# Kernel tuning notes

Measured on AMD Instinct MI355X. Metric: run time of the kernel, lower is better.

## Reference

```python
import jax, jax.numpy as jnp
import numpy as np

B, S, I, H = 32, 512, 512, 1024

def _xavier(key, shape):
    fan_in, fan_out = shape[0], shape[1]
    a = jnp.sqrt(6.0 / (fan_in + fan_out))
    return jax.random.uniform(key, shape, jnp.float32, -a, a)

def setup_inputs() -> dict:
    key = jax.random.key(0)
    ks = jax.random.split(key, 10)
    inp = {
        'x': jax.random.normal(ks[0], (B, S, I), jnp.float32),
        'h0': jnp.zeros((B, H), jnp.float32),
        'c0': jnp.zeros((B, H), jnp.float32),
        'W_ii': _xavier(ks[1], (I, H)), 'W_hi': _xavier(ks[2], (H, H)), 'b_i': jnp.zeros((H,), jnp.float32),
        'W_if': _xavier(ks[3], (I, H)), 'W_hf': _xavier(ks[4], (H, H)), 'b_f': jnp.zeros((H,), jnp.float32),
        'W_ig': _xavier(ks[5], (I, H)), 'W_hg': _xavier(ks[6], (H, H)), 'b_g': jnp.zeros((H,), jnp.float32),
        'W_io': _xavier(ks[7], (I, H)), 'W_ho': _xavier(ks[8], (H, H)), 'b_o': jnp.zeros((H,), jnp.float32),
    }
    return inp

def _lstm(x, h0, c0, W_ii, W_hi, b_i, W_if, W_hf, b_f, W_ig, W_hg, b_g, W_io, W_ho, b_o):
    # Precompute input-to-hidden projections for all timesteps (big fused GEMMs).
    xi = jnp.einsum('bsi,ih->sbh', x, W_ii) + b_i  # (S,B,H)
    xf = jnp.einsum('bsi,ih->sbh', x, W_if) + b_f
    xg = jnp.einsum('bsi,ih->sbh', x, W_ig) + b_g
    xo = jnp.einsum('bsi,ih->sbh', x, W_io) + b_o

    def step(carry, gates_t):
        h, c = carry
        xi_t, xf_t, xg_t, xo_t = gates_t
        i_t = jax.nn.sigmoid(xi_t + h @ W_hi)
        f_t = jax.nn.sigmoid(xf_t + h @ W_hf)
        g_t = jnp.tanh(xg_t + h @ W_hg)
        o_t = jax.nn.sigmoid(xo_t + h @ W_ho)
        c_new = f_t * c + i_t * g_t
        h_new = o_t * jnp.tanh(c_new)
        return (h_new, c_new), (h_new, f_t, i_t, o_t, g_t, c_new)

    (hT, cT), (hs, fs, is_, os, gs, cs) = jax.lax.scan(step, (h0, c0), (xi, xf, xg, xo))
    hidden_seq = jnp.transpose(hs, (1, 0, 2))  # (B,S,H)
    return hidden_seq, hT, cT, fs, is_, os, gs, cs

def reference(x, h0, c0, W_ii, W_hi, b_i, W_if, W_hf, b_f, W_ig, W_hg, b_g, W_io, W_ho, b_o):
    return _lstm(x, h0, c0, W_ii, W_hi, b_i, W_if, W_hf, b_f, W_ig, W_hg, b_g, W_io, W_ho, b_o)
```

## Files before the change

kernel.cpp:

```cpp
#include <hip/hip_runtime.h>
#include <stdint.h>

#define S_LEN 512
#define BATCH 32
#define IDIM 512
#define HDIM 1024
#define NBLK 64

typedef __attribute__((ext_vector_type(8))) short bf16x8;
typedef __attribute__((ext_vector_type(4))) float f32x4;

typedef const __attribute__((address_space(1))) unsigned int as1_uint;
typedef __attribute__((address_space(3))) unsigned int as3_uint;

__device__ __forceinline__ unsigned short f2bf(float f) {
  unsigned int u = __float_as_uint(f);
  u = (u + 0x7fffu + ((u >> 16) & 1u)) >> 16;
  return (unsigned short)u;
}

__device__ __forceinline__ void gld_lds16(const void* g, void* l) {
  __builtin_amdgcn_global_load_lds((as1_uint*)g, (as3_uint*)l, 16, 0, 0);
}

__device__ __forceinline__ float sigm(float x) { return 1.f / (1.f + __expf(-x)); }
__device__ __forceinline__ float tanh_f(float x) { return 1.f - 2.f / (__expf(2.f * x) + 1.f); }

__global__ void k_cast_x(const float* __restrict__ src, unsigned short* __restrict__ dst, int n8) {
  int i0 = blockIdx.x * blockDim.x + threadIdx.x;
  int stride = gridDim.x * blockDim.x;
  for (int i = i0; i < n8; i += stride) {
    const float4* s4 = (const float4*)(src + (size_t)i * 8);
    float4 a = s4[0], b = s4[1];
    bf16x8 v;
    v[0] = (short)f2bf(a.x); v[1] = (short)f2bf(a.y); v[2] = (short)f2bf(a.z); v[3] = (short)f2bf(a.w);
    v[4] = (short)f2bf(b.x); v[5] = (short)f2bf(b.y); v[6] = (short)f2bf(b.z); v[7] = (short)f2bf(b.w);
    *(bf16x8*)(dst + (size_t)i * 8) = v;
  }
}

__global__ void k_tcast_w(const float* __restrict__ src, unsigned short* __restrict__ dst, int K) {
  __shared__ float t[64][65];
  int k0 = blockIdx.x * 64, h0 = blockIdx.y * 64;
  int tid = threadIdx.x;
#pragma unroll 4
  for (int j = 0; j < 16; ++j) {
    int idx = j * 256 + tid;
    int kl = idx >> 6, hl = idx & 63;
    t[kl][hl] = src[(size_t)(k0 + kl) * HDIM + h0 + hl];
  }
  __syncthreads();
  int hl = tid >> 2, kg = tid & 3;
  unsigned short* drow = dst + (size_t)(h0 + hl) * K + k0 + kg * 16;
#pragma unroll
  for (int jj = 0; jj < 4; ++jj) {
    ushort4 v;
    v.x = f2bf(t[kg * 16 + jj * 4 + 0][hl]);
    v.y = f2bf(t[kg * 16 + jj * 4 + 1][hl]);
    v.z = f2bf(t[kg * 16 + jj * 4 + 2][hl]);
    v.w = f2bf(t[kg * 16 + jj * 4 + 3][hl]);
    *(ushort4*)(drow + jj * 4) = v;
  }
}

__global__ __launch_bounds__(256) void k_proj(
    const unsigned short* __restrict__ xb, const unsigned short* __restrict__ wib,
    const float* __restrict__ b_i, const float* __restrict__ b_f,
    const float* __restrict__ b_g, const float* __restrict__ b_o,
    float* __restrict__ Xi, float* __restrict__ Xf, float* __restrict__ Xg,
    float* __restrict__ Xo) {
  __shared__ unsigned short As[128 * 64];
  __shared__ unsigned short Bs[128 * 64];
  int tid = threadIdx.x;
  int l = tid & 63, w = tid >> 6;
  int mt = blockIdx.x >> 5, nt = blockIdx.x & 31;
  int m0 = mt * 128, n0 = nt * 128;
  int g = nt >> 3;
  int wm = (w >> 1) * 64, wn = (w & 1) * 64;

  f32x4 acc[4][4];
  for (int mi = 0; mi < 4; ++mi)
    for (int ni = 0; ni < 4; ++ni)
      for (int r = 0; r < 4; ++r) acc[mi][ni][r] = 0.f;

  for (int kt = 0; kt < 8; ++kt) {
    int k0 = kt * 64;
#pragma unroll
    for (int j = 0; j < 4; ++j) {
      int idx = j * 256 + tid;
      int row = idx >> 3, c = idx & 7;
      int sc = c ^ (row & 7);
      gld_lds16(xb + (size_t)(m0 + row) * IDIM + k0 + sc * 8,
                (char*)As + ((j * 256 + (w << 6)) << 4));
      gld_lds16(wib + (size_t)(n0 + row) * IDIM + k0 + sc * 8,
                (char*)Bs + ((j * 256 + (w << 6)) << 4));
    }
    __syncthreads();
#pragma unroll
    for (int kst = 0; kst < 2; ++kst) {
      bf16x8 af[4], bfr[4];
#pragma unroll
      for (int mi = 0; mi < 4; ++mi) {
        int row = wm + mi * 16 + (l & 15);
        int c = (kst << 2) + (l >> 4);
        af[mi] = *(const bf16x8*)((const char*)As + row * 128 + ((c ^ (row & 7)) << 4));
      }
#pragma unroll
      for (int ni = 0; ni < 4; ++ni) {
        int row = wn + ni * 16 + (l & 15);
        int c = (kst << 2) + (l >> 4);
        bfr[ni] = *(const bf16x8*)((const char*)Bs + row * 128 + ((c ^ (row & 7)) << 4));
      }
#pragma unroll
      for (int mi = 0; mi < 4; ++mi)
#pragma unroll
        for (int ni = 0; ni < 4; ++ni)
          acc[mi][ni] = __builtin_amdgcn_mfma_f32_16x16x32_bf16(af[mi], bfr[ni], acc[mi][ni], 0, 0, 0);
    }
    __syncthreads();
  }

  const float* bias = g == 0 ? b_i : g == 1 ? b_f : g == 2 ? b_g : b_o;
  float* dst = g == 0 ? Xi : g == 1 ? Xf : g == 2 ? Xg : Xo;
#pragma unroll
  for (int ni = 0; ni < 4; ++ni) {
    int n = n0 + wn + ni * 16 + (l & 15);
    int h = n & 1023;
    float bv = bias[h];
#pragma unroll
    for (int mi = 0; mi < 4; ++mi)
#pragma unroll
      for (int r = 0; r < 4; ++r) {
        int m = m0 + wm + mi * 16 + ((l >> 4) << 2) + r;
        int b = m >> 9, s = m & 511;
        dst[(size_t)(s * BATCH + b) * HDIM + h] = acc[mi][ni][r] + bv;
      }
  }
}

__global__ __launch_bounds__(256, 1) void k_rnn(
    const unsigned short* __restrict__ whb, const float* __restrict__ h0,
    const float* __restrict__ c0, char* __restrict__ hbufA,
    char* __restrict__ hbufB, unsigned int* __restrict__ cnt,
    const float* __restrict__ Xi, const float* __restrict__ Xf,
    const float* __restrict__ Xg, const float* __restrict__ Xo,
    float* __restrict__ csw, float* __restrict__ hseq, float* __restrict__ hT,
    float* __restrict__ cT) {
  __shared__ char lds[41472];
  const int ACT = 32768;

  const int tid = threadIdx.x;
  const int w = tid >> 6, l = tid & 63;
  const int ln = l & 15, lk = l >> 4;
  const int bid = blockIdx.x;
  const int dm = bid & 1, hb = bid >> 1;

  float* isw = (float*)Xi; float* fsw = (float*)Xf;
  float* gsw = (float*)Xg; float* osw = (float*)Xo;
  const float* XW = (w == 0) ? Xi : (w == 1) ? Xf : (w == 2) ? Xg : Xo;

  bf16x8 Breg[8][8];
#pragma unroll
  for (int g = 0; g < 4; ++g)
#pragma unroll
    for (int hh = 0; hh < 2; ++hh)
#pragma unroll
      for (int j = 0; j < 8; ++j) {
        const size_t row = (size_t)((g << 10) + (hb << 5) + (hh << 4) + ln);
        Breg[g * 2 + hh][j] =
            *(const bf16x8*)(whb + (row << 10) + (w << 8) + (j << 5) + (lk << 3));
      }
#pragma unroll
  for (int nt = 0; nt < 8; ++nt)
#pragma unroll
    for (int j = 0; j < 8; ++j)
      asm volatile("" : "+a"(Breg[nt][j]));

  const int pb = tid >> 4, hp = tid & 15;
  const int bg = (dm << 4) + pb;
  const int gh = (hb << 5) + (hp << 1);
  const int o = hp << 1;
  const int foff = (dm << 15) + (hb << 10) + ((o >> 3) << 8) + (pb << 4) + ((o & 7) << 1);
  unsigned int* const myflag = cnt + (((dm << 2) + (hb & 3)) << 5);

  float2 c = *(const float2*)&c0[((size_t)bg << 10) + gh];

  {
    float2 hv = *(const float2*)&h0[((size_t)bg << 10) + gh];
    unsigned int pv = (unsigned int)f2bf(hv.x) | ((unsigned int)f2bf(hv.y) << 16);
    __hip_atomic_store((unsigned int*)(hbufA + foff), pv, __ATOMIC_RELAXED,
                       __HIP_MEMORY_SCOPE_AGENT);
    asm volatile("s_waitcnt vmcnt(0)" ::: "memory");
    __syncthreads();
    if (tid == 0)
      __hip_atomic_fetch_add(myflag, 1u, __ATOMIC_RELAXED, __HIP_MEMORY_SCOPE_AGENT);
  }

  for (int t = 0; t < S_LEN; ++t) {
    const char* hin = (t & 1) ? hbufB : hbufA;
    char* hout = (t & 1) ? hbufA : hbufB;

    float xp[2][4];
    {
      const float* xb_ = XW + ((size_t)((t << 5) + (dm << 4)) << 10) + (hb << 5) + ln;
#pragma unroll
      for (int hh = 0; hh < 2; ++hh)
#pragma unroll
        for (int r = 0; r < 4; ++r)
          xp[hh][r] = xb_[((size_t)((lk << 2) + r) << 10) + (hh << 4)];
    }

    {
      const unsigned int need = 8u * (unsigned int)(t + 1);
      const unsigned int* cp = cnt + (((dm << 2) + (l & 3)) << 5);
      while (true) {
        unsigned int v = __hip_atomic_load(cp, __ATOMIC_RELAXED, __HIP_MEMORY_SCOPE_AGENT);
        if (__all((l < 4) ? (int)(v >= need) : 1)) break;
        __builtin_amdgcn_s_sleep(1);
      }
    }
    __builtin_amdgcn_sched_barrier(0);

    bf16x8 a[8];
    const char* abase = hin + (dm << 15);
#pragma unroll
    for (int j = 0; j < 8; ++j) {
      const char* ap = abase + (((w << 3) + j) << 10) + (l << 4);
      asm volatile("global_load_dwordx4 %0, %1, off sc0 sc1"
                   : "=v"(a[j]) : "v"(ap) : "memory");
    }
    asm volatile("s_waitcnt vmcnt(0)" ::: "memory");
    __builtin_amdgcn_sched_barrier(0);

    f32x4 acc[8];
#pragma unroll
    for (int nt = 0; nt < 8; ++nt)
#pragma unroll
      for (int r = 0; r < 4; ++r) acc[nt][r] = 0.f;
#pragma unroll
    for (int j = 0; j < 8; ++j)
#pragma unroll
      for (int nt = 0; nt < 8; ++nt)
        acc[nt] = __builtin_amdgcn_mfma_f32_16x16x32_bf16(a[j], Breg[nt][j], acc[nt], 0, 0, 0);

#pragma unroll
    for (int nt = 0; nt < 8; ++nt)
      *(f32x4*)(lds + (((w << 3) + nt) << 10) + (l << 4)) = acc[nt];
    __syncthreads();

#pragma unroll
    for (int hh = 0; hh < 2; ++hh) {
      const int nt = (w << 1) + hh;
      f32x4 s = *(const f32x4*)(lds + (nt << 10) + (l << 4));
#pragma unroll
      for (int kw = 1; kw < 4; ++kw) {
        f32x4 p = *(const f32x4*)(lds + (((kw << 3) + nt) << 10) + (l << 4));
#pragma unroll
        for (int r = 0; r < 4; ++r) s[r] += p[r];
      }
#pragma unroll
      for (int r = 0; r < 4; ++r) {
        float pre = s[r] + xp[hh][r];
        float act = (w == 2) ? tanh_f(pre) : sigm(pre);
        ((float*)(lds + ACT))[((w << 4) + (lk << 2) + r) * 34 + (hh << 4) + ln] = act;
      }
    }
    __syncthreads();

    const float* af = (const float*)(lds + ACT);
    float2 iv = *(const float2*)&af[(0 * 16 + pb) * 34 + o];
    float2 fv = *(const float2*)&af[(1 * 16 + pb) * 34 + o];
    float2 gv = *(const float2*)&af[(2 * 16 + pb) * 34 + o];
    float2 ov = *(const float2*)&af[(3 * 16 + pb) * 34 + o];

    c.x = fv.x * c.x + iv.x * gv.x;
    c.y = fv.y * c.y + iv.y * gv.y;
    float h0v = ov.x * tanh_f(c.x), h1v = ov.y * tanh_f(c.y);

    if (t < S_LEN - 1) {
      unsigned int pv = (unsigned int)f2bf(h0v) | ((unsigned int)f2bf(h1v) << 16);
      __hip_atomic_store((unsigned int*)(hout + foff), pv, __ATOMIC_RELAXED,
                         __HIP_MEMORY_SCOPE_AGENT);
      asm volatile("s_waitcnt vmcnt(0)" ::: "memory");
      __syncthreads();
      if (tid == 0)
        __hip_atomic_fetch_add(myflag, 1u, __ATOMIC_RELAXED, __HIP_MEMORY_SCOPE_AGENT);
    }

    size_t oo = ((size_t)((t << 5) + bg) << 10) + gh;
    *(float2*)(isw + oo) = iv;
    *(float2*)(fsw + oo) = fv;
    *(float2*)(gsw + oo) = gv;
    *(float2*)(osw + oo) = ov;
    *(float2*)(csw + oo) = c;
    *(float2*)(hseq + (((size_t)(bg << 9) + t) << 10) + gh) = make_float2(h0v, h1v);
    if (t == S_LEN - 1) {
      *(float2*)(hT + ((size_t)bg << 10) + gh) = make_float2(h0v, h1v);
      *(float2*)(cT + ((size_t)bg << 10) + gh) = c;
    }
  }
}

extern "C" void kernel_launch(void* const* d_in, const int* in_sizes, int n_in,
                              void* d_out, int out_size, void* d_ws, size_t ws_size,
                              hipStream_t stream) {
  const float* x = (const float*)d_in[0];
  const float* h0 = (const float*)d_in[1];
  const float* c0 = (const float*)d_in[2];
  const float* Wi[4] = {(const float*)d_in[3], (const float*)d_in[6], (const float*)d_in[9], (const float*)d_in[12]};
  const float* Wh[4] = {(const float*)d_in[4], (const float*)d_in[7], (const float*)d_in[10], (const float*)d_in[13]};
  const float* bias[4] = {(const float*)d_in[5], (const float*)d_in[8], (const float*)d_in[11], (const float*)d_in[14]};

  float* out = (float*)d_out;
  float* R0 = out;
  float* R1 = out + 16777216;
  float* R2 = R1 + 32768;
  float* R3 = R2 + 32768;
  float* R4 = R3 + 16777216;
  float* R5 = R4 + 16777216;
  float* R6 = R5 + 16777216;
  float* R7 = R6 + 16777216;
  float* Xg_[4] = {R4, R3, R6, R5};

  char* ws = (char*)d_ws;
  unsigned short* whb = (unsigned short*)ws;
  unsigned short* wib = (unsigned short*)(ws + 8388608);
  char* hbufA = ws + 12582912;
  char* hbufB = ws + 12648448;
  unsigned int* cnt = (unsigned int*)(ws + 12713984);

  unsigned short* xb = (unsigned short*)R0;

  hipMemsetAsync(cnt, 0, 1024, stream);
  k_cast_x<<<2048, 256, 0, stream>>>(x, xb, (BATCH * S_LEN * IDIM) / 8);
  for (int g = 0; g < 4; ++g) {
    k_tcast_w<<<dim3(8, 16), 256, 0, stream>>>(Wi[g], wib + (size_t)g * 1024 * 512, 512);
    k_tcast_w<<<dim3(16, 16), 256, 0, stream>>>(Wh[g], whb + (size_t)g * 1024 * 1024, 1024);
  }
  k_proj<<<4096, 256, 0, stream>>>(xb, wib, bias[0], bias[1], bias[2], bias[3],
                                   Xg_[0], Xg_[1], Xg_[2], Xg_[3]);
  k_rnn<<<NBLK, 256, 0, stream>>>(whb, h0, c0, hbufA, hbufB, cnt,
                                  Xg_[0], Xg_[1], Xg_[2], Xg_[3],
                                  R7, R0, R1, R2);
}
```

Measured before the change: 1.945 ms.

## Replace counter-flag barrier with tagged hidden-state publishing for step sync

Each thread now writes its bf16 hidden pair together with a 32-bit step tag in a single 64-bit atomic store. Consumers spin by reloading the whole h slice and checking the tags, so the data load also serves as the readiness check. This removes the per-block s_waitcnt, __syncthreads, atomic counter increment and separate polling loop on the recurrent critical path. In exchange each step moves twice the h data and consumers repeatedly reload the full slice while waiting. The hx buffer reuses the wib region in the workspace and is cleared after the projection kernel has finished with it.

```diff
diff --git a/kernel.cpp b/kernel.cpp
--- a/kernel.cpp
+++ b/kernel.cpp
@@ -6,9 +6,11 @@
 #define IDIM 512
 #define HDIM 1024
 #define NBLK 64
+#define TAGB 0xC0DE0000u
 
 typedef __attribute__((ext_vector_type(8))) short bf16x8;
 typedef __attribute__((ext_vector_type(4))) float f32x4;
+typedef __attribute__((ext_vector_type(4))) unsigned int u32x4;
 
 typedef const __attribute__((address_space(1))) unsigned int as1_uint;
 typedef __attribute__((address_space(3))) unsigned int as3_uint;
@@ -25,6 +27,10 @@
 
 __device__ __forceinline__ float sigm(float x) { return 1.f / (1.f + __expf(-x)); }
 __device__ __forceinline__ float tanh_f(float x) { return 1.f - 2.f / (__expf(2.f * x) + 1.f); }
+
+#define LDX4(dst, addr, OFF)                                             \
+  asm volatile("global_load_dwordx4 %0, %1, off offset:" #OFF " sc0 sc1" \
+               : "=v"(dst) : "v"(addr) : "memory")
 
 __global__ void k_cast_x(const float* __restrict__ src, unsigned short* __restrict__ dst, int n8) {
   int i0 = blockIdx.x * blockDim.x + threadIdx.x;
@@ -140,8 +146,7 @@
 
 __global__ __launch_bounds__(256, 1) void k_rnn(
     const unsigned short* __restrict__ whb, const float* __restrict__ h0,
-    const float* __restrict__ c0, char* __restrict__ hbufA,
-    char* __restrict__ hbufB, unsigned int* __restrict__ cnt,
+    const float* __restrict__ c0, char* __restrict__ hx,
     const float* __restrict__ Xi, const float* __restrict__ Xf,
     const float* __restrict__ Xg, const float* __restrict__ Xo,
     float* __restrict__ csw, float* __restrict__ hseq, float* __restrict__ hT,
@@ -180,26 +185,21 @@
   const int bg = (dm << 4) + pb;
   const int gh = (hb << 5) + (hp << 1);
   const int o = hp << 1;
-  const int foff = (dm << 15) + (hb << 10) + ((o >> 3) << 8) + (pb << 4) + ((o & 7) << 1);
-  unsigned int* const myflag = cnt + (((dm << 2) + (hb & 3)) << 5);
+  char* const pub = hx + (dm << 16) + (pb << 12) + (((hb << 4) + hp) << 3);
+  const char* const cons = hx + (dm << 16) + (ln << 12) + (w << 10) + (lk << 5);
 
   float2 c = *(const float2*)&c0[((size_t)bg << 10) + gh];
 
   {
     float2 hv = *(const float2*)&h0[((size_t)bg << 10) + gh];
-    unsigned int pv = (unsigned int)f2bf(hv.x) | ((unsigned int)f2bf(hv.y) << 16);
-    __hip_atomic_store((unsigned int*)(hbufA + foff), pv, __ATOMIC_RELAXED,
+    unsigned long long pv =
+        (unsigned long long)((unsigned int)f2bf(hv.x) | ((unsigned int)f2bf(hv.y) << 16)) |
+        ((unsigned long long)TAGB << 32);
+    __hip_atomic_store((unsigned long long*)pub, pv, __ATOMIC_RELAXED,
                        __HIP_MEMORY_SCOPE_AGENT);
-    asm volatile("s_waitcnt vmcnt(0)" ::: "memory");
-    __syncthreads();
-    if (tid == 0)
-      __hip_atomic_fetch_add(myflag, 1u, __ATOMIC_RELAXED, __HIP_MEMORY_SCOPE_AGENT);
   }
 
   for (int t = 0; t < S_LEN; ++t) {
-    const char* hin = (t & 1) ? hbufB : hbufA;
-    char* hout = (t & 1) ? hbufA : hbufB;
-
     float xp[2][4];
     {
       const float* xb_ = XW + ((size_t)((t << 5) + (dm << 4)) << 10) + (hb << 5) + ln;
@@ -210,27 +210,35 @@
           xp[hh][r] = xb_[((size_t)((lk << 2) + r) << 10) + (hh << 4)];
     }
 
-    {
-      const unsigned int need = 8u * (unsigned int)(t + 1);
-      const unsigned int* cp = cnt + (((dm << 2) + (l & 3)) << 5);
-      while (true) {
-        unsigned int v = __hip_atomic_load(cp, __ATOMIC_RELAXED, __HIP_MEMORY_SCOPE_AGENT);
-        if (__all((l < 4) ? (int)(v >= need) : 1)) break;
-        __builtin_amdgcn_s_sleep(1);
-      }
-    }
-    __builtin_amdgcn_sched_barrier(0);
+    const char* ab = cons + ((t & 1) << 17);
+    const unsigned int want = TAGB + (unsigned int)t;
+    u32x4 raw[16];
+    while (true) {
+      LDX4(raw[0], ab, 0);    LDX4(raw[1], ab, 16);
+      LDX4(raw[2], ab, 128);  LDX4(raw[3], ab, 144);
+      LDX4(raw[4], ab, 256);  LDX4(raw[5], ab, 272);
+      LDX4(raw[6], ab, 384);  LDX4(raw[7], ab, 400);
+      LDX4(raw[8], ab, 512);  LDX4(raw[9], ab, 528);
+      LDX4(raw[10], ab, 640); LDX4(raw[11], ab, 656);
+      LDX4(raw[12], ab, 768); LDX4(raw[13], ab, 784);
+      LDX4(raw[14], ab, 896); LDX4(raw[15], ab, 912);
+      asm volatile("s_waitcnt vmcnt(0)" ::: "memory");
+      __builtin_amdgcn_sched_barrier(0);
+      unsigned int ok = 1;
+#pragma unroll
+      for (int i = 0; i < 16; ++i)
+        ok &= (unsigned int)(raw[i][1] == want) & (unsigned int)(raw[i][3] == want);
+      if (__all((int)ok)) break;
+    }
 
     bf16x8 a[8];
-    const char* abase = hin + (dm << 15);
 #pragma unroll
     for (int j = 0; j < 8; ++j) {
-      const char* ap = abase + (((w << 3) + j) << 10) + (l << 4);
-      asm volatile("global_load_dwordx4 %0, %1, off sc0 sc1"
-                   : "=v"(a[j]) : "v"(ap) : "memory");
-    }
-    asm volatile("s_waitcnt vmcnt(0)" ::: "memory");
-    __builtin_amdgcn_sched_barrier(0);
+      u32x4 t4;
+      t4[0] = raw[2 * j][0]; t4[1] = raw[2 * j][2];
+      t4[2] = raw[2 * j + 1][0]; t4[3] = raw[2 * j + 1][2];
+      a[j] = __builtin_bit_cast(bf16x8, t4);
+    }
 
     f32x4 acc[8];
 #pragma unroll
@@ -278,13 +286,11 @@
     float h0v = ov.x * tanh_f(c.x), h1v = ov.y * tanh_f(c.y);
 
     if (t < S_LEN - 1) {
-      unsigned int pv = (unsigned int)f2bf(h0v) | ((unsigned int)f2bf(h1v) << 16);
-      __hip_atomic_store((unsigned int*)(hout + foff), pv, __ATOMIC_RELAXED,
-                         __HIP_MEMORY_SCOPE_AGENT);
-      asm volatile("s_waitcnt vmcnt(0)" ::: "memory");
-      __syncthreads();
-      if (tid == 0)
-        __hip_atomic_fetch_add(myflag, 1u, __ATOMIC_RELAXED, __HIP_MEMORY_SCOPE_AGENT);
+      unsigned long long pv =
+          (unsigned long long)((unsigned int)f2bf(h0v) | ((unsigned int)f2bf(h1v) << 16)) |
+          ((unsigned long long)(TAGB + (unsigned int)(t + 1)) << 32);
+      __hip_atomic_store((unsigned long long*)(pub + ((~t & 1) << 17)), pv,
+                         __ATOMIC_RELAXED, __HIP_MEMORY_SCOPE_AGENT);
     }
 
     size_t oo = ((size_t)((t << 5) + bg) << 10) + gh;
@@ -325,13 +331,10 @@
   char* ws = (char*)d_ws;
   unsigned short* whb = (unsigned short*)ws;
   unsigned short* wib = (unsigned short*)(ws + 8388608);
-  char* hbufA = ws + 12582912;
-  char* hbufB = ws + 12648448;
-  unsigned int* cnt = (unsigned int*)(ws + 12713984);
+  char* hx = ws + 8388608;
 
   unsigned short* xb = (unsigned short*)R0;
 
-  hipMemsetAsync(cnt, 0, 1024, stream);
   k_cast_x<<<2048, 256, 0, stream>>>(x, xb, (BATCH * S_LEN * IDIM) / 8);
   for (int g = 0; g < 4; ++g) {
     k_tcast_w<<<dim3(8, 16), 256, 0, stream>>>(Wi[g], wib + (size_t)g * 1024 * 512, 512);
@@ -339,7 +342,8 @@
   }
   k_proj<<<4096, 256, 0, stream>>>(xb, wib, bias[0], bias[1], bias[2], bias[3],
                                    Xg_[0], Xg_[1], Xg_[2], Xg_[3]);
-  k_rnn<<<NBLK, 256, 0, stream>>>(whb, h0, c0, hbufA, hbufB, cnt,
+  hipMemsetAsync(hx, 0, 262144, stream);
+  k_rnn<<<NBLK, 256, 0, stream>>>(whb, h0, c0, hx,
                                   Xg_[0], Xg_[1], Xg_[2], Xg_[3],
                                   R7, R0, R1, R2);
 }
```

Result: slower. 2.687 ms (+38.2%).

## Signal per-wave readiness and defer per-step output stores past the h fetch

Applied to the files above, without the earlier changes.

Drops the block-wide barrier before signalling that h is ready. Each wave now bumps the ready counter itself after its own store completes, and the wait threshold rises from 8 to 32 per step to match. The gate and state output stores for step t are deferred into step t+1, issued after the h operand loads, and the XW prefetch moves after them. The aim is to take the output write traffic and the barrier off the recurrent critical path. In exchange there are four times as many atomic increments per step, and the vmcnt(0) waits may now cover the deferred stores.

```diff
diff --git a/kernel.cpp b/kernel.cpp
--- a/kernel.cpp
+++ b/kernel.cpp
@@ -185,14 +185,16 @@
 
   float2 c = *(const float2*)&c0[((size_t)bg << 10) + gh];
 
+  float2 piv, pfv, pgv, pov, pc;
+  float ph0 = 0.f, ph1 = 0.f;
+
   {
     float2 hv = *(const float2*)&h0[((size_t)bg << 10) + gh];
     unsigned int pv = (unsigned int)f2bf(hv.x) | ((unsigned int)f2bf(hv.y) << 16);
     __hip_atomic_store((unsigned int*)(hbufA + foff), pv, __ATOMIC_RELAXED,
                        __HIP_MEMORY_SCOPE_AGENT);
     asm volatile("s_waitcnt vmcnt(0)" ::: "memory");
-    __syncthreads();
-    if (tid == 0)
+    if (l == 0)
       __hip_atomic_fetch_add(myflag, 1u, __ATOMIC_RELAXED, __HIP_MEMORY_SCOPE_AGENT);
   }
 
@@ -200,18 +202,8 @@
     const char* hin = (t & 1) ? hbufB : hbufA;
     char* hout = (t & 1) ? hbufA : hbufB;
 
-    float xp[2][4];
     {
-      const float* xb_ = XW + ((size_t)((t << 5) + (dm << 4)) << 10) + (hb << 5) + ln;
-#pragma unroll
-      for (int hh = 0; hh < 2; ++hh)
-#pragma unroll
-        for (int r = 0; r < 4; ++r)
-          xp[hh][r] = xb_[((size_t)((lk << 2) + r) << 10) + (hh << 4)];
-    }
-
-    {
-      const unsigned int need = 8u * (unsigned int)(t + 1);
+      const unsigned int need = 32u * (unsigned int)(t + 1);
       const unsigned int* cp = cnt + (((dm << 2) + (l & 3)) << 5);
       while (true) {
         unsigned int v = __hip_atomic_load(cp, __ATOMIC_RELAXED, __HIP_MEMORY_SCOPE_AGENT);
@@ -232,6 +224,26 @@
     asm volatile("s_waitcnt vmcnt(0)" ::: "memory");
     __builtin_amdgcn_sched_barrier(0);
 
+    if (t > 0) {
+      size_t po = ((size_t)(((t - 1) << 5) + bg) << 10) + gh;
+      *(float2*)(isw + po) = piv;
+      *(float2*)(fsw + po) = pfv;
+      *(float2*)(gsw + po) = pgv;
+      *(float2*)(osw + po) = pov;
+      *(float2*)(csw + po) = pc;
+      *(float2*)(hseq + (((size_t)(bg << 9) + (t - 1)) << 10) + gh) = make_float2(ph0, ph1);
+    }
+
+    float xp[2][4];
+    {
+      const float* xb_ = XW + ((size_t)((t << 5) + (dm << 4)) << 10) + (hb << 5) + ln;
+#pragma unroll
+      for (int hh = 0; hh < 2; ++hh)
+#pragma unroll
+        for (int r = 0; r < 4; ++r)
+          xp[hh][r] = xb_[((size_t)((lk << 2) + r) << 10) + (hh << 4)];
+    }
+
     f32x4 acc[8];
 #pragma unroll
     for (int nt = 0; nt < 8; ++nt)
@@ -282,22 +294,23 @@
       __hip_atomic_store((unsigned int*)(hout + foff), pv, __ATOMIC_RELAXED,
                          __HIP_MEMORY_SCOPE_AGENT);
       asm volatile("s_waitcnt vmcnt(0)" ::: "memory");
-      __syncthreads();
-      if (tid == 0)
+      if (l == 0)
         __hip_atomic_fetch_add(myflag, 1u, __ATOMIC_RELAXED, __HIP_MEMORY_SCOPE_AGENT);
     }
 
-    size_t oo = ((size_t)((t << 5) + bg) << 10) + gh;
-    *(float2*)(isw + oo) = iv;
-    *(float2*)(fsw + oo) = fv;
-    *(float2*)(gsw + oo) = gv;
-    *(float2*)(osw + oo) = ov;
-    *(float2*)(csw + oo) = c;
-    *(float2*)(hseq + (((size_t)(bg << 9) + t) << 10) + gh) = make_float2(h0v, h1v);
-    if (t == S_LEN - 1) {
-      *(float2*)(hT + ((size_t)bg << 10) + gh) = make_float2(h0v, h1v);
-      *(float2*)(cT + ((size_t)bg << 10) + gh) = c;
-    }
+    piv = iv; pfv = fv; pgv = gv; pov = ov; pc = c; ph0 = h0v; ph1 = h1v;
+  }
+
+  {
+    size_t po = ((size_t)(((S_LEN - 1) << 5) + bg) << 10) + gh;
+    *(float2*)(isw + po) = piv;
+    *(float2*)(fsw + po) = pfv;
+    *(float2*)(gsw + po) = pgv;
+    *(float2*)(osw + po) = pov;
+    *(float2*)(csw + po) = pc;
+    *(float2*)(hseq + (((size_t)(bg << 9) + (S_LEN - 1)) << 10) + gh) = make_float2(ph0, ph1);
+    *(float2*)(hT + ((size_t)bg << 10) + gh) = make_float2(ph0, ph1);
+    *(float2*)(cT + ((size_t)bg << 10) + gh) = pc;
   }
 }
 
```

Result: slower. 2.372 ms (+21.9%).

## Replace atomic counters with per-block step flags and pipeline h loads into MFMAs

Applied to the files above, without the earlier changes.

Each block now stores its own step number into a dedicated slot instead of doing atomic fetch-adds on 4 shared counters, and every lane of a wave polls one flag. This is meant to remove atomic contention and shorten the cross-block barrier in the recurrent loop. The h-vector loads are also drained incrementally with staged vmcnt waits, so MFMAs for early chunks start before later loads arrive. The x-projection loads become inline asm so they are not reordered. The risk is that the vmcnt counting now depends on the exact ordering of outstanding loads, including the asm x loads issued earlier.

```diff
diff --git a/kernel.cpp b/kernel.cpp
--- a/kernel.cpp
+++ b/kernel.cpp
@@ -141,7 +141,7 @@
 __global__ __launch_bounds__(256, 1) void k_rnn(
     const unsigned short* __restrict__ whb, const float* __restrict__ h0,
     const float* __restrict__ c0, char* __restrict__ hbufA,
-    char* __restrict__ hbufB, unsigned int* __restrict__ cnt,
+    char* __restrict__ hbufB, unsigned int* __restrict__ sent,
     const float* __restrict__ Xi, const float* __restrict__ Xf,
     const float* __restrict__ Xg, const float* __restrict__ Xo,
     float* __restrict__ csw, float* __restrict__ hseq, float* __restrict__ hT,
@@ -181,7 +181,8 @@
   const int gh = (hb << 5) + (hp << 1);
   const int o = hp << 1;
   const int foff = (dm << 15) + (hb << 10) + ((o >> 3) << 8) + (pb << 4) + ((o & 7) << 1);
-  unsigned int* const myflag = cnt + (((dm << 2) + (hb & 3)) << 5);
+  unsigned int* const smy = sent + (dm << 7) + ((hb >> 3) << 5) + ((hb & 7) << 2);
+  const unsigned int* const spoll = sent + (dm << 7) + (w << 5) + ((l & 7) << 2);
 
   float2 c = *(const float2*)&c0[((size_t)bg << 10) + gh];
 
@@ -193,7 +194,7 @@
     asm volatile("s_waitcnt vmcnt(0)" ::: "memory");
     __syncthreads();
     if (tid == 0)
-      __hip_atomic_fetch_add(myflag, 1u, __ATOMIC_RELAXED, __HIP_MEMORY_SCOPE_AGENT);
+      __hip_atomic_store(smy, 1u, __ATOMIC_RELAXED, __HIP_MEMORY_SCOPE_AGENT);
   }
 
   for (int t = 0; t < S_LEN; ++t) {
@@ -206,16 +207,18 @@
 #pragma unroll
       for (int hh = 0; hh < 2; ++hh)
 #pragma unroll
-        for (int r = 0; r < 4; ++r)
-          xp[hh][r] = xb_[((size_t)((lk << 2) + r) << 10) + (hh << 4)];
+        for (int r = 0; r < 4; ++r) {
+          const float* xa = xb_ + (((size_t)((lk << 2) + r)) << 10) + (hh << 4);
+          asm volatile("global_load_dword %0, %1, off"
+                       : "=v"(xp[hh][r]) : "v"(xa) : "memory");
+        }
     }
 
     {
-      const unsigned int need = 8u * (unsigned int)(t + 1);
-      const unsigned int* cp = cnt + (((dm << 2) + (l & 3)) << 5);
+      const unsigned int need = (unsigned int)(t + 1);
       while (true) {
-        unsigned int v = __hip_atomic_load(cp, __ATOMIC_RELAXED, __HIP_MEMORY_SCOPE_AGENT);
-        if (__all((l < 4) ? (int)(v >= need) : 1)) break;
+        unsigned int v = __hip_atomic_load(spoll, __ATOMIC_RELAXED, __HIP_MEMORY_SCOPE_AGENT);
+        if (__all((int)(v >= need))) break;
         __builtin_amdgcn_s_sleep(1);
       }
     }
@@ -229,19 +232,26 @@
       asm volatile("global_load_dwordx4 %0, %1, off sc0 sc1"
                    : "=v"(a[j]) : "v"(ap) : "memory");
     }
-    asm volatile("s_waitcnt vmcnt(0)" ::: "memory");
-    __builtin_amdgcn_sched_barrier(0);
-
     f32x4 acc[8];
 #pragma unroll
     for (int nt = 0; nt < 8; ++nt)
 #pragma unroll
       for (int r = 0; r < 4; ++r) acc[nt][r] = 0.f;
-#pragma unroll
-    for (int j = 0; j < 8; ++j)
-#pragma unroll
-      for (int nt = 0; nt < 8; ++nt)
-        acc[nt] = __builtin_amdgcn_mfma_f32_16x16x32_bf16(a[j], Breg[nt][j], acc[nt], 0, 0, 0);
+
+#define STAGE(J, CNT)                                                        \
+    asm volatile("s_waitcnt vmcnt(" #CNT ")" ::: "memory");                  \
+    __builtin_amdgcn_sched_barrier(0);                                       \
+    acc[0] = __builtin_amdgcn_mfma_f32_16x16x32_bf16(a[J], Breg[0][J], acc[0], 0, 0, 0); \
+    acc[1] = __builtin_amdgcn_mfma_f32_16x16x32_bf16(a[J], Breg[1][J], acc[1], 0, 0, 0); \
+    acc[2] = __builtin_amdgcn_mfma_f32_16x16x32_bf16(a[J], Breg[2][J], acc[2], 0, 0, 0); \
+    acc[3] = __builtin_amdgcn_mfma_f32_16x16x32_bf16(a[J], Breg[3][J], acc[3], 0, 0, 0); \
+    acc[4] = __builtin_amdgcn_mfma_f32_16x16x32_bf16(a[J], Breg[4][J], acc[4], 0, 0, 0); \
+    acc[5] = __builtin_amdgcn_mfma_f32_16x16x32_bf16(a[J], Breg[5][J], acc[5], 0, 0, 0); \
+    acc[6] = __builtin_amdgcn_mfma_f32_16x16x32_bf16(a[J], Breg[6][J], acc[6], 0, 0, 0); \
+    acc[7] = __builtin_amdgcn_mfma_f32_16x16x32_bf16(a[J], Breg[7][J], acc[7], 0, 0, 0);
+    STAGE(0, 7) STAGE(1, 6) STAGE(2, 5) STAGE(3, 4)
+    STAGE(4, 3) STAGE(5, 2) STAGE(6, 1) STAGE(7, 0)
+#undef STAGE
 
 #pragma unroll
     for (int nt = 0; nt < 8; ++nt)
@@ -284,7 +294,8 @@
       asm volatile("s_waitcnt vmcnt(0)" ::: "memory");
       __syncthreads();
       if (tid == 0)
-        __hip_atomic_fetch_add(myflag, 1u, __ATOMIC_RELAXED, __HIP_MEMORY_SCOPE_AGENT);
+        __hip_atomic_store(smy, (unsigned int)(t + 2), __ATOMIC_RELAXED,
+                           __HIP_MEMORY_SCOPE_AGENT);
     }
 
     size_t oo = ((size_t)((t << 5) + bg) << 10) + gh;
@@ -327,11 +338,11 @@
   unsigned short* wib = (unsigned short*)(ws + 8388608);
   char* hbufA = ws + 12582912;
   char* hbufB = ws + 12648448;
-  unsigned int* cnt = (unsigned int*)(ws + 12713984);
+  unsigned int* sent = (unsigned int*)(ws + 12713984);
 
   unsigned short* xb = (unsigned short*)R0;
 
-  hipMemsetAsync(cnt, 0, 1024, stream);
+  hipMemsetAsync(sent, 0, 1024, stream);
   k_cast_x<<<2048, 256, 0, stream>>>(x, xb, (BATCH * S_LEN * IDIM) / 8);
   for (int g = 0; g < 4; ++g) {
     k_tcast_w<<<dim3(8, 16), 256, 0, stream>>>(Wi[g], wib + (size_t)g * 1024 * 512, 512);
@@ -339,7 +350,7 @@
   }
   k_proj<<<4096, 256, 0, stream>>>(xb, wib, bias[0], bias[1], bias[2], bias[3],
                                    Xg_[0], Xg_[1], Xg_[2], Xg_[3]);
-  k_rnn<<<NBLK, 256, 0, stream>>>(whb, h0, c0, hbufA, hbufB, cnt,
+  k_rnn<<<NBLK, 256, 0, stream>>>(whb, h0, c0, hbufA, hbufB, sent,
                                   Xg_[0], Xg_[1], Xg_[2], Xg_[3],
                                   R7, R0, R1, R2);
 }
```

Measured after the change: 1.890 ms, median of 2. 2.8% less time.
